# Performance work log

Measured on AMD Instinct MI355X. Metric: run time of the kernel, lower is better.

Reference implementation:

```python
import jax, jax.numpy as jnp
import numpy as np

B, N, D, HID, OUT = 4, 6144, 64, 512, 64
FINE_CONF = 0.25


def setup_inputs() -> dict:
    key = jax.random.key(0)
    ks = jax.random.split(key, 16)

    def unit(k, shape):
        v = jax.random.normal(k, shape, dtype=jnp.float32)
        return v / jnp.linalg.norm(v, axis=-1, keepdims=True)

    def lin(k, fan_in, shape):
        return jax.random.normal(k, shape, dtype=jnp.float32) * (1.0 / np.sqrt(fan_in))

    return {
        'feats1': unit(ks[0], (B, N, D)),
        'feats2': unit(ks[1], (B, N, D)),
        'kps1': jax.random.uniform(ks[2], (B, N, 2), dtype=jnp.float32) * 512.0,
        'kps2': jax.random.uniform(ks[3], (B, N, 2), dtype=jnp.float32) * 512.0,
        'scales1': jnp.ones((B, N), dtype=jnp.float32),
        'w1': lin(ks[4], 2 * D, (2 * D, HID)), 'b1': jnp.zeros((HID,), jnp.float32),
        'w2': lin(ks[5], HID, (HID, HID)),   'b2': jnp.zeros((HID,), jnp.float32),
        'w3': lin(ks[6], HID, (HID, HID)),   'b3': jnp.zeros((HID,), jnp.float32),
        'w4': lin(ks[7], HID, (HID, HID)),   'b4': jnp.zeros((HID,), jnp.float32),
        'w5': lin(ks[8], HID, (HID, OUT)),   'b5': jnp.zeros((OUT,), jnp.float32),
    }


def _fine_matcher(x, w1, b1, w2, b2, w3, b3, w4, b4, w5, b5):
    # eval-mode BN folded into the Linears -> plain MLP
    h = jax.nn.relu(x @ w1 + b1)
    h = jax.nn.relu(h @ w2 + b2)
    h = jax.nn.relu(h @ w3 + b3)
    h = jax.nn.relu(h @ w4 + b4)
    return h @ w5 + b5  # [B, N, 64]


def reference(feats1, feats2, kps1, kps2, scales1,
              w1, b1, w2, b2, w3, b3, w4, b4, w5, b5):
    # ---- batch_match: dense cosine sim + bidirectional argmax + mutual check ----
    cossim = jnp.einsum('bnd,bmd->bnm', feats1, feats2)       # [B, N, N]
    match12 = jnp.argmax(cossim, axis=-1)                      # [B, N]
    match21 = jnp.argmax(cossim, axis=1)                       # [B, N] (argmax over rows)
    idx0 = jnp.arange(match12.shape[1])
    back = jnp.take_along_axis(match21, match12, axis=1)       # match21[match12]
    mutual = back == idx0[None, :]                             # [B, N] bool

    # ---- refine_matches (masked instead of boolean compaction, jit-friendly) ----
    f2 = jnp.take_along_axis(feats2, match12[..., None], axis=1)   # [B, N, D]
    mkpts1 = jnp.take_along_axis(kps2, match12[..., None], axis=1) # [B, N, 2]
    offsets_raw = _fine_matcher(jnp.concatenate([feats1, f2], axis=-1),
                                w1, b1, w2, b2, w3, b3, w4, b4, w5, b5)  # [B, N, 64]

    # conf = softmax(3*offsets).max ; subpix uses softmax(3*offsets) too (temp=3)
    heat = jax.nn.softmax(3.0 * offsets_raw, axis=-1)          # [B, N, 64]
    conf = jnp.max(heat, axis=-1)                              # [B, N]

    hm = heat.reshape(heat.shape[0], heat.shape[1], 8, 8)      # [B, N, Hh, Wh]
    g = jnp.arange(8, dtype=heat.dtype) - 4.0                  # x - W//2 / y - H//2
    coords_x = jnp.sum(hm * g[None, None, None, :], axis=(-1, -2))
    coords_y = jnp.sum(hm * g[None, None, :, None], axis=(-1, -2))
    offsets = jnp.stack([coords_x, coords_y], axis=-1)         # [B, N, 2]

    mkpts0 = kps1 + offsets * scales1[..., None]
    matches = jnp.concatenate([mkpts0, mkpts1], axis=-1)       # [B, N, 4]
    mask_good = mutual & (conf > FINE_CONF)                    # valid-match mask
    return matches, mask_good
```

## Files before the change

kernel.cpp:

```cpp
#include <hip/hip_runtime.h>
#include <cstddef>
#include <cstdint>

#define BB 4
#define NN 6144
#define DD 64
#define HID 512
#define OUTD 64
#define CAP 512
#define RSPLIT 8

typedef unsigned long long ull;
typedef unsigned int u32;
typedef unsigned short u16;
typedef unsigned char u8;
typedef __attribute__((ext_vector_type(8))) short short8_t;
typedef __attribute__((ext_vector_type(4))) float floatx4;

#define OFF_ROWFIN 0
#define OFF_COLFIN 196608
#define OFF_WT     393216
#define OFF_F1T    2162688
#define OFF_F2T    5308416
#define OFF_RBM    8454144
#define OFF_CBM    10813440
#define OFF_CNTR   13172736
#define OFF_CNTC   13173504
#define OFF_LISTR  13174272
#define OFF_LISTC  13567488

#define WT1_OFF 0
#define WT2_OFF 65536
#define WT3_OFF 327680
#define WT4_OFF 589824
#define WT5_OFF 851968
#define WT_TOTAL 884736

__device__ __forceinline__ unsigned int fkey(float v) {
    unsigned int u = __float_as_uint(v);
    return (u & 0x80000000u) ? ~u : (u | 0x80000000u);
}

__device__ __forceinline__ float inv16(u32 k16) {
    u32 u = k16 << 16;
    return (u & 0x80000000u) ? __uint_as_float(u & 0x7fffffffu)
                             : __uint_as_float(~u);
}

__device__ __forceinline__ u16 f2bf(float f) {
    unsigned int u = __float_as_uint(f);
    u += 0x7FFFu + ((u >> 16) & 1u);
    return (u16)(u >> 16);
}

__device__ __forceinline__ u32 f2fp8x2(float a, float b) {
    return (u32)__builtin_amdgcn_cvt_pk_fp8_f32(a, b, 0, false) & 0xffffu;
}

__global__ __launch_bounds__(256) void prep_kernel(
    const float* __restrict__ w1, const float* __restrict__ w2,
    const float* __restrict__ w3, const float* __restrict__ w4,
    const float* __restrict__ w5,
    const float* __restrict__ f1, const float* __restrict__ f2,
    u8* __restrict__ wt8, u16* __restrict__ f1t, u16* __restrict__ f2t,
    ull* __restrict__ finals, int* __restrict__ cnts)
{
    int idx = blockIdx.x * 256 + threadIdx.x;

    if (idx < 2 * BB * NN) finals[idx] = 0ULL;
    if (idx < 384) cnts[idx] = 0;

    if (idx < WT_TOTAL) {
        const float* w; u8* o; int K, nsh, li;
        if (idx < 65536)        { w = w1; o = wt8 + WT1_OFF; K = 128; nsh = 9; li = idx; }
        else if (idx < 327680)  { w = w2; o = wt8 + WT2_OFF; K = 512; nsh = 9; li = idx - 65536; }
        else if (idx < 589824)  { w = w3; o = wt8 + WT3_OFF; K = 512; nsh = 9; li = idx - 327680; }
        else if (idx < 851968)  { w = w4; o = wt8 + WT4_OFF; K = 512; nsh = 9; li = idx - 589824; }
        else                    { w = w5; o = wt8 + WT5_OFF; K = 512; nsh = 6; li = idx - 851968; }
        int k = li >> nsh;
        int n = li & ((1 << nsh) - 1);
        u8 v = (u8)(f2fp8x2(w[li], 0.0f) & 0xff);
        int lane = (n & 15) | (((k >> 3) & 3) << 4);
        o[(((size_t)(n >> 4) * (K >> 5) + (k >> 5)) * 64 + lane) * 8 + (k & 7)] = v;
    }

    {
        const int TE = BB * NN * DD;
        const float* src; u16* dst; int e;
        if (idx < TE) { src = f1; dst = f1t; e = idx; }
        else          { src = f2; dst = f2t; e = idx - TE; }
        int k  = e & 63;
        int rn = e >> 6;
        int b  = rn / NN;
        int r  = rn - b * NN;
        int R  = r >> 7, rb = (r >> 4) & 7;
        int kb = k >> 5, lane = (r & 15) | (((k >> 3) & 3) << 4), j = k & 7;
        dst[(size_t)(b * 48 + R) * 8192 + ((rb * 2 + kb) * 64 + lane) * 8 + j] = f2bf(src[e]);
    }
}

__global__ __launch_bounds__(256, 4) void simb_kernel(
    const u16* __restrict__ f1t, const u16* __restrict__ f2t,
    u16* __restrict__ rbm, u16* __restrict__ cbm)
{
    __shared__ __align__(16) u16 sA[8192];
    __shared__ __align__(16) u16 sB[8192];
    __shared__ float cv[4][128];
    const int R = blockIdx.x, C = blockIdx.y, b = blockIdx.z;
    const int t = threadIdx.x, lane = t & 63, w = t >> 6;
    const int l15 = lane & 15, l4 = lane >> 4;

    const u16* Ag = f1t + (size_t)(b * 48 + R) * 8192;
    const u16* Bg = f2t + (size_t)(b * 48 + C) * 8192;

    #pragma unroll
    for (int rnd = 0; rnd < 4; ++rnd) {
        int c = rnd * 256 + t;
        *reinterpret_cast<uint4*>(&sA[c * 8]) = *reinterpret_cast<const uint4*>(Ag + c * 8);
        *reinterpret_cast<uint4*>(&sB[c * 8]) = *reinterpret_cast<const uint4*>(Bg + c * 8);
    }
    __syncthreads();

    floatx4 acc[2][8];
    #pragma unroll
    for (int i = 0; i < 2; ++i)
        #pragma unroll
        for (int j = 0; j < 8; ++j) acc[i][j] = (floatx4)(0.0f);

    #pragma unroll
    for (int kb = 0; kb < 2; ++kb) {
        short8_t afr[2];
        #pragma unroll
        for (int i = 0; i < 2; ++i)
            afr[i] = *reinterpret_cast<const short8_t*>(
                &sA[(((2 * w + i) * 2 + kb) * 64 + lane) * 8]);
        #pragma unroll
        for (int j = 0; j < 8; ++j) {
            short8_t bfr = *reinterpret_cast<const short8_t*>(
                &sB[((j * 2 + kb) * 64 + lane) * 8]);
            #pragma unroll
            for (int i = 0; i < 2; ++i)
                acc[i][j] = __builtin_amdgcn_mfma_f32_16x16x32_bf16(
                    afr[i], bfr, acc[i][j], 0, 0, 0);
        }
    }

    #pragma unroll
    for (int i = 0; i < 2; ++i) {
        #pragma unroll
        for (int reg = 0; reg < 4; ++reg) {
            float v = acc[i][0][reg];
            #pragma unroll
            for (int j = 1; j < 8; ++j) v = fmaxf(v, acc[i][j][reg]);
            v = fmaxf(v, __shfl_xor(v, 1));
            v = fmaxf(v, __shfl_xor(v, 2));
            v = fmaxf(v, __shfl_xor(v, 4));
            v = fmaxf(v, __shfl_xor(v, 8));
            if (l15 == 0) {
                int row = R * 128 + w * 32 + i * 16 + l4 * 4 + reg;
                rbm[((size_t)b * 48 + C) * NN + row] = (u16)(fkey(v) >> 16);
            }
        }
    }

    #pragma unroll
    for (int j = 0; j < 8; ++j) {
        float v = acc[0][j][0];
        #pragma unroll
        for (int i = 0; i < 2; ++i)
            #pragma unroll
            for (int reg = 0; reg < 4; ++reg) v = fmaxf(v, acc[i][j][reg]);
        v = fmaxf(v, __shfl_xor(v, 16));
        v = fmaxf(v, __shfl_xor(v, 32));
        if (l4 == 0) cv[w][j * 16 + l15] = v;
    }
    __syncthreads();
    if (t < 128) {
        float v = fmaxf(fmaxf(cv[0][t], cv[1][t]), fmaxf(cv[2][t], cv[3][t]));
        cbm[((size_t)b * 48 + R) * NN + C * 128 + t] = (u16)(fkey(v) >> 16);
    }
}

__global__ __launch_bounds__(256) void scan_kernel(
    const u16* __restrict__ rbm, const u16* __restrict__ cbm,
    int* __restrict__ cntR, int* __restrict__ cntC,
    int* __restrict__ listR, int* __restrict__ listC)
{
    const u16* bm = blockIdx.y ? cbm : rbm;
    int* cnt  = blockIdx.y ? cntC : cntR;
    int* list = blockIdx.y ? listC : listR;

    __shared__ int lcnt[48];
    __shared__ int lbase[48];
    const int t = threadIdx.x;
    if (t < 48) lcnt[t] = 0;
    const int idx = blockIdx.x * 256 + t;
    const int b = (blockIdx.x * 256) / NN;
    const int n = idx - b * NN;

    u16 ks[48];
    #pragma unroll
    for (int c = 0; c < 48; ++c)
        ks[c] = bm[((size_t)b * 48 + c) * NN + n];

    u16 mx = 0;
    #pragma unroll
    for (int c = 0; c < 48; ++c) mx = ks[c] > mx ? ks[c] : mx;
    float thr = inv16(mx) - 0.010f;
    u32 m0 = 0, m1 = 0;
    #pragma unroll
    for (int c = 0; c < 48; ++c) {
        if (inv16((u32)ks[c] + 1) >= thr) {
            if (c < 32) m0 |= 1u << c; else m1 |= 1u << (c - 32);
        }
    }
    __syncthreads();
    {
        u32 a = m0;
        while (a) { int c = __builtin_ctz(a); a &= a - 1; atomicAdd(&lcnt[c], 1); }
        a = m1;
        while (a) { int c = 32 + __builtin_ctz(a); a &= a - 1; atomicAdd(&lcnt[c], 1); }
    }
    __syncthreads();
    if (t < 48) { lbase[t] = atomicAdd(&cnt[b * 48 + t], lcnt[t]); lcnt[t] = 0; }
    __syncthreads();
    {
        u32 a = m0;
        while (a) {
            int c = __builtin_ctz(a); a &= a - 1;
            int pos = lbase[c] + atomicAdd(&lcnt[c], 1);
            if (pos < CAP) list[(b * 48 + c) * CAP + pos] = n;
        }
        a = m1;
        while (a) {
            int c = 32 + __builtin_ctz(a); a &= a - 1;
            int pos = lbase[c] + atomicAdd(&lcnt[c], 1);
            if (pos < CAP) list[(b * 48 + c) * CAP + pos] = n;
        }
    }
}

__global__ __launch_bounds__(256, 2) void refine_kernel(
    const float* __restrict__ f1, const float* __restrict__ f2,
    const int* __restrict__ cntR, const int* __restrict__ cntC,
    const int* __restrict__ listR, const int* __restrict__ listC,
    ull* __restrict__ rowfin, ull* __restrict__ colfin)
{
    const float* qfeat = blockIdx.z ? f2 : f1;
    const float* tfeat = blockIdx.z ? f1 : f2;
    const int* cnt  = blockIdx.z ? cntC : cntR;
    const int* list = blockIdx.z ? listC : listR;
    ull* fin = blockIdx.z ? colfin : rowfin;

    const int b = blockIdx.x / 48;
    const int C = blockIdx.x - b * 48;
    const int sub = blockIdx.y;
    int n_items = cnt[b * 48 + C];
    if (n_items > CAP) n_items = CAP;
    int chunk = (n_items + RSPLIT - 1) / RSPLIT;
    int lo = sub * chunk;
    int hi = lo + chunk; if (hi > n_items) hi = n_items;
    if (lo >= hi) return;

    __shared__ float s2f[128 * 68];
    __shared__ float sq[16 * 68];
    const int t = threadIdx.x;
    const float* tb = tfeat + ((size_t)b * NN + C * 128) * 64;
    #pragma unroll
    for (int p = 0; p < 8; ++p) {
        int idx = p * 256 + t;
        int row = idx >> 4, c4 = idx & 15;
        *reinterpret_cast<float4*>(&s2f[row * 68 + c4 * 4]) =
            *reinterpret_cast<const float4*>(tb + row * 64 + c4 * 4);
    }
    __syncthreads();
    const int rs = t >> 4, cg = t & 15;
    const int* mylist = list + (b * 48 + C) * CAP;
    for (int base = lo; base < hi; base += 16) {
        {
            int lq = base + rs;
            int nn = (lq < hi) ? mylist[lq] : mylist[lo];
            *reinterpret_cast<float4*>(&sq[rs * 68 + cg * 4]) =
                *reinterpret_cast<const float4*>(qfeat + ((size_t)b * NN + nn) * 64 + cg * 4);
        }
        __syncthreads();

        int li = base + rs;
        bool valid = li < hi;
        int n = valid ? mylist[li] : mylist[lo];
        float dot[8];
        #pragma unroll
        for (int c8 = 0; c8 < 8; ++c8) dot[c8] = 0.0f;
        #pragma unroll 4
        for (int kq = 0; kq < 16; ++kq) {
            float4 a4 = *reinterpret_cast<const float4*>(&sq[rs * 68 + kq * 4]);
            #pragma unroll
            for (int c8 = 0; c8 < 8; ++c8) {
                float4 s4 = *reinterpret_cast<const float4*>(&s2f[(cg + 16 * c8) * 68 + kq * 4]);
                dot[c8] = fmaf(a4.x, s4.x, dot[c8]);
                dot[c8] = fmaf(a4.y, s4.y, dot[c8]);
                dot[c8] = fmaf(a4.z, s4.z, dot[c8]);
                dot[c8] = fmaf(a4.w, s4.w, dot[c8]);
            }
        }
        float bv = dot[0]; int bc = cg;
        #pragma unroll
        for (int c8 = 1; c8 < 8; ++c8) {
            if (dot[c8] > bv) { bv = dot[c8]; bc = cg + 16 * c8; }
        }
        ull pk = ((ull)fkey(bv) << 32) | (u32)(~(u32)(C * 128 + bc));
        ull qq;
        qq = __shfl_xor(pk, 1); pk = pk > qq ? pk : qq;
        qq = __shfl_xor(pk, 2); pk = pk > qq ? pk : qq;
        qq = __shfl_xor(pk, 4); pk = pk > qq ? pk : qq;
        qq = __shfl_xor(pk, 8); pk = pk > qq ? pk : qq;
        if (cg == 0 && valid) atomicMax(&fin[(size_t)b * NN + n], pk);
        __syncthreads();
    }
}


#define MLP_STEP(BUF, KB)                                                        \
    {                                                                            \
        const int kb2 = ((KB) + woff) & (NKB - 1);                               \
        __builtin_amdgcn_s_setprio(1);                                           \
        _Pragma("unroll")                                                        \
        for (int jb = 0; jb < 6; ++jb) {                                         \
            const int pt = jb * 16 + l15;                                        \
            const int sp = (kb2 * 4 + l4) ^ (pt & 7);                            \
            long bfr = *reinterpret_cast<const long*>(act + pt * 512 + sp * 8);  \
            _Pragma("unroll")                                                    \
            for (int ia = 0; ia < 4; ++ia)                                       \
                acc[ia][jb] = __builtin_amdgcn_mfma_f32_16x16x32_fp8_fp8(        \
                    BUF[ia], bfr, acc[ia][jb], 0, 0, 0);                         \
        }                                                                        \
        __builtin_amdgcn_s_setprio(0);                                           \
        if ((KB) + 3 < NKB) {                                                    \
            const int kbp = ((KB) + 3 + woff) & (NKB - 1);                       \
            _Pragma("unroll")                                                    \
            for (int ia = 0; ia < 4; ++ia)                                       \
                BUF[ia] = *reinterpret_cast<const long*>(                        \
                    wt8 + (((size_t)(chBlk0 + ia) * NKB + kbp) * 64 + lane) * 8);\
        }                                                                        \
    }

template<int K>
__device__ __forceinline__ void mlp_layer8(
    u8* act, const u8* __restrict__ wt8,
    const float* __restrict__ bias, int lane, int wid)
{
    constexpr int NKB = K / 32;
    floatx4 acc[4][6];
    #pragma unroll
    for (int ia = 0; ia < 4; ++ia)
        #pragma unroll
        for (int jb = 0; jb < 6; ++jb)
            acc[ia][jb] = (floatx4)(0.0f);

    const int l15 = lane & 15, l4 = lane >> 4;
    const int chBlk0 = wid * 4;
    const int woff = (wid * 2) & (NKB - 1);

    long a0[4], a1[4], a2[4];
    #pragma unroll
    for (int ia = 0; ia < 4; ++ia)
        a0[ia] = *reinterpret_cast<const long*>(
            wt8 + (((size_t)(chBlk0 + ia) * NKB + ((0 + woff) & (NKB - 1))) * 64 + lane) * 8);
    #pragma unroll
    for (int ia = 0; ia < 4; ++ia)
        a1[ia] = *reinterpret_cast<const long*>(
            wt8 + (((size_t)(chBlk0 + ia) * NKB + ((1 + woff) & (NKB - 1))) * 64 + lane) * 8);
    #pragma unroll
    for (int ia = 0; ia < 4; ++ia)
        a2[ia] = *reinterpret_cast<const long*>(
            wt8 + (((size_t)(chBlk0 + ia) * NKB + ((2 + woff) & (NKB - 1))) * 64 + lane) * 8);

    #pragma unroll
    for (int kb = 0; kb < NKB; ++kb) {
        if ((kb % 3) == 0)      MLP_STEP(a0, kb)
        else if ((kb % 3) == 1) MLP_STEP(a1, kb)
        else                    MLP_STEP(a2, kb)
    }
    __syncthreads();

    const int ch0 = wid * 64;
    #pragma unroll
    for (int ia = 0; ia < 4; ++ia) {
        int cb = ia * 16 + l4 * 4;
        float4 bv = *reinterpret_cast<const float4*>(bias + ch0 + cb);
        #pragma unroll
        for (int jb = 0; jb < 6; ++jb) {
            int pt = jb * 16 + l15;
            u32 pk0 = f2fp8x2(fmaxf(acc[ia][jb][0] + bv.x, 0.0f),
                              fmaxf(acc[ia][jb][1] + bv.y, 0.0f));
            u32 pk1 = f2fp8x2(fmaxf(acc[ia][jb][2] + bv.z, 0.0f),
                              fmaxf(acc[ia][jb][3] + bv.w, 0.0f));
            u32 word = pk0 | (pk1 << 16);
            int s = (ch0 + cb) >> 3;
            int sp = s ^ (pt & 7);
            *reinterpret_cast<u32*>(act + pt * 512 + sp * 8 + (cb & 4)) = word;
        }
    }
    __syncthreads();
}

__global__ __launch_bounds__(512, 2) void mlp_mfma_kernel(
    const float* __restrict__ f1, const float* __restrict__ f2,
    const float* __restrict__ kps1, const float* __restrict__ kps2,
    const float* __restrict__ scales1,
    const float* __restrict__ b1, const float* __restrict__ b2,
    const float* __restrict__ b3, const float* __restrict__ b4,
    const float* __restrict__ b5,
    const u8* __restrict__ wt8,
    const ull* __restrict__ rowfin, const ull* __restrict__ colfin,
    float* __restrict__ out)
{
    __shared__ __align__(16) unsigned char lds_raw[49152];
    u8* act = lds_raw;
    float* logf = reinterpret_cast<float*>(lds_raw);

    const int t = threadIdx.x;
    const int lane = t & 63, wid = t >> 6;
    const int base = blockIdx.x * 96;
    const int b = base / NN;
    const int n0 = base % NN;

    if (t < 384) {
        const int pt = t >> 2, seg = t & 3;
        const int n = n0 + pt;
        ull rm = rowfin[(size_t)b * NN + n];
        const int m = (int)(~(u32)(rm & 0xffffffffULL));
        const float* src = (seg < 2)
            ? (f1 + ((size_t)b * NN + n) * DD + seg * 32)
            : (f2 + ((size_t)b * NN + m) * DD + (seg - 2) * 32);
        #pragma unroll
        for (int q8 = 0; q8 < 4; ++q8) {
            float4 v0 = *reinterpret_cast<const float4*>(src + q8 * 8);
            float4 v1 = *reinterpret_cast<const float4*>(src + q8 * 8 + 4);
            ull w64 = (ull)f2fp8x2(v0.x, v0.y)
                    | ((ull)f2fp8x2(v0.z, v0.w) << 16)
                    | ((ull)f2fp8x2(v1.x, v1.y) << 32)
                    | ((ull)f2fp8x2(v1.z, v1.w) << 48);
            int s = seg * 4 + q8;
            int sp = s ^ (pt & 7);
            *reinterpret_cast<ull*>(act + pt * 512 + sp * 8) = w64;
        }
    }
    __syncthreads();

    mlp_layer8<128>(act, wt8 + WT1_OFF, b1, lane, wid);
    mlp_layer8<512>(act, wt8 + WT2_OFF, b2, lane, wid);
    mlp_layer8<512>(act, wt8 + WT3_OFF, b3, lane, wid);
    mlp_layer8<512>(act, wt8 + WT4_OFF, b4, lane, wid);

    {
        const int l15 = lane & 15, l4 = lane >> 4;
        floatx4 acc5[6];
        #pragma unroll
        for (int jb = 0; jb < 6; ++jb) acc5[jb] = (floatx4)(0.0f);
        if (wid < 4) {
            const int woff5 = (wid * 4) & 15;
            long a_cur = *reinterpret_cast<const long*>(
                wt8 + WT5_OFF + (((size_t)wid * 16 + woff5) * 64 + lane) * 8);
            long a_nxt;
            #pragma unroll
            for (int kb = 0; kb < 16; ++kb) {
                const int kb2 = (kb + woff5) & 15;
                if (kb + 1 < 16) {
                    const int kbn = (kb + 1 + woff5) & 15;
                    a_nxt = *reinterpret_cast<const long*>(
                        wt8 + WT5_OFF + (((size_t)wid * 16 + kbn) * 64 + lane) * 8);
                }
                __builtin_amdgcn_s_setprio(1);
                #pragma unroll
                for (int jb = 0; jb < 6; ++jb) {
                    const int pt = jb * 16 + l15;
                    const int sp = (kb2 * 4 + l4) ^ (pt & 7);
                    long bfr = *reinterpret_cast<const long*>(act + pt * 512 + sp * 8);
                    acc5[jb] = __builtin_amdgcn_mfma_f32_16x16x32_fp8_fp8(
                        a_cur, bfr, acc5[jb], 0, 0, 0);
                }
                __builtin_amdgcn_s_setprio(0);
                if (kb + 1 < 16) a_cur = a_nxt;
            }
        }
        __syncthreads();
        if (wid < 4) {
            int cb = wid * 16 + l4 * 4;
            float4 bv = *reinterpret_cast<const float4*>(b5 + cb);
            #pragma unroll
            for (int jb = 0; jb < 6; ++jb) {
                int pt = jb * 16 + l15;
                float4 o;
                o.x = acc5[jb][0] + bv.x;
                o.y = acc5[jb][1] + bv.y;
                o.z = acc5[jb][2] + bv.z;
                o.w = acc5[jb][3] + bv.w;
                *reinterpret_cast<float4*>(&logf[pt * 68 + cb]) = o;
            }
        }
        __syncthreads();
    }

    if (t < 96) {
        const int pt = t;
        const int n = n0 + pt;
        const float* lrow = &logf[pt * 68];
        float mx = -1e30f;
        #pragma unroll 8
        for (int j = 0; j < OUTD; ++j) mx = fmaxf(mx, 3.0f * lrow[j]);
        float s = 0.0f, cx = 0.0f, cy = 0.0f;
        #pragma unroll 8
        for (int j = 0; j < OUTD; ++j) {
            float e = __expf(3.0f * lrow[j] - mx);
            s  += e;
            cx += e * (float)((j & 7) - 4);
            cy += e * (float)((j >> 3) - 4);
        }
        float conf = 1.0f / s;
        cx /= s; cy /= s;
        ull rm = rowfin[(size_t)b * NN + n];
        int m = (int)(~(u32)(rm & 0xffffffffULL));
        ull cm = colfin[(size_t)b * NN + m];
        int back = (int)(~(u32)(cm & 0xffffffffULL));
        bool mutual = (back == n);
        float sc = scales1[(size_t)b * NN + n];
        float x0 = kps1[((size_t)b * NN + n) * 2 + 0] + cx * sc;
        float y0 = kps1[((size_t)b * NN + n) * 2 + 1] + cy * sc;
        float x1 = kps2[((size_t)b * NN + m) * 2 + 0];
        float y1 = kps2[((size_t)b * NN + m) * 2 + 1];
        float* mt = out + ((size_t)b * NN + n) * 4;
        mt[0] = x0; mt[1] = y0; mt[2] = x1; mt[3] = y1;
        out[(size_t)BB * NN * 4 + (size_t)b * NN + n] =
            (mutual && conf > 0.25f) ? 1.0f : 0.0f;
    }
}

extern "C" void kernel_launch(void* const* d_in, const int* in_sizes, int n_in,
                              void* d_out, int out_size, void* d_ws, size_t ws_size,
                              hipStream_t stream)
{
    const float* f1  = (const float*)d_in[0];
    const float* f2  = (const float*)d_in[1];
    const float* kp1 = (const float*)d_in[2];
    const float* kp2 = (const float*)d_in[3];
    const float* sc1 = (const float*)d_in[4];
    const float* w1  = (const float*)d_in[5];
    const float* b1  = (const float*)d_in[6];
    const float* w2  = (const float*)d_in[7];
    const float* b2  = (const float*)d_in[8];
    const float* w3  = (const float*)d_in[9];
    const float* b3  = (const float*)d_in[10];
    const float* w4  = (const float*)d_in[11];
    const float* b4  = (const float*)d_in[12];
    const float* w5  = (const float*)d_in[13];
    const float* b5  = (const float*)d_in[14];

    char* ws = (char*)d_ws;
    ull* rowfin = (ull*)(ws + OFF_ROWFIN);
    ull* colfin = (ull*)(ws + OFF_COLFIN);
    u8*  wt8    = (u8*)(ws + OFF_WT);
    u16* f1t    = (u16*)(ws + OFF_F1T);
    u16* f2t    = (u16*)(ws + OFF_F2T);
    u16* rbm    = (u16*)(ws + OFF_RBM);
    u16* cbm    = (u16*)(ws + OFF_CBM);
    int* cntR   = (int*)(ws + OFF_CNTR);
    int* cntC   = (int*)(ws + OFF_CNTC);
    int* listR  = (int*)(ws + OFF_LISTR);
    int* listC  = (int*)(ws + OFF_LISTC);
    float* out  = (float*)d_out;

    prep_kernel<<<(2 * BB * NN * DD) / 256, 256, 0, stream>>>(
        w1, w2, w3, w4, w5, f1, f2, wt8, f1t, f2t, rowfin, cntR);

    dim3 gS(48, 48, BB);
    simb_kernel<<<gS, 256, 0, stream>>>(f1t, f2t, rbm, cbm);

    dim3 gScan((BB * NN) / 256, 2);
    scan_kernel<<<gScan, 256, 0, stream>>>(rbm, cbm, cntR, cntC, listR, listC);

    dim3 gR(BB * 48, RSPLIT, 2);
    refine_kernel<<<gR, 256, 0, stream>>>(f1, f2, cntR, cntC, listR, listC,
                                          rowfin, colfin);

    mlp_mfma_kernel<<<(BB * NN) / 96, 512, 0, stream>>>(
        f1, f2, kp1, kp2, sc1, b1, b2, b3, b4, b5, wt8, rowfin, colfin, out);
}
```

Measured before the change: 139.9 us.

## Register-tile candidate refinement kernel and reduce row split factor

The refinement kernel, which recomputes exact fp32 argmax over a 128-column chunk for listed candidate rows, no longer stages the 128 target rows in shared memory. Each thread now computes a 4x4 register tile (4 queries by 4 targets), reading target vectors directly from global/L2, over 32 queries per iteration. RSPLIT drops from 8 to 2, so fewer blocks each handle more items and the per-block target load is amortized differently. This trades shared-memory staging and LDS bandwidth for more global loads of the target tile and fewer launched blocks, which may reduce parallelism.

```diff
diff --git a/kernel.cpp b/kernel.cpp
--- a/kernel.cpp
+++ b/kernel.cpp
@@ -8,7 +8,7 @@
 #define HID 512
 #define OUTD 64
 #define CAP 512
-#define RSPLIT 8
+#define RSPLIT 2
 
 typedef unsigned long long ull;
 typedef unsigned int u32;
@@ -262,60 +262,76 @@
     int hi = lo + chunk; if (hi > n_items) hi = n_items;
     if (lo >= hi) return;
 
-    __shared__ float s2f[128 * 68];
-    __shared__ float sq[16 * 68];
+    __shared__ float sq[32 * 64];
     const int t = threadIdx.x;
+    const int tq = t & 31;
+    const int qg = t >> 5;
     const float* tb = tfeat + ((size_t)b * NN + C * 128) * 64;
-    #pragma unroll
-    for (int p = 0; p < 8; ++p) {
-        int idx = p * 256 + t;
-        int row = idx >> 4, c4 = idx & 15;
-        *reinterpret_cast<float4*>(&s2f[row * 68 + c4 * 4]) =
-            *reinterpret_cast<const float4*>(tb + row * 64 + c4 * 4);
-    }
-    __syncthreads();
-    const int rs = t >> 4, cg = t & 15;
     const int* mylist = list + (b * 48 + C) * CAP;
-    for (int base = lo; base < hi; base += 16) {
-        {
-            int lq = base + rs;
+
+    for (int base = lo; base < hi; base += 32) {
+        __syncthreads();
+        #pragma unroll
+        for (int s = 0; s < 2; ++s) {
+            int fi = s * 256 + t;
+            int q = fi >> 4, c4 = fi & 15;
+            int lq = base + q;
             int nn = (lq < hi) ? mylist[lq] : mylist[lo];
-            *reinterpret_cast<float4*>(&sq[rs * 68 + cg * 4]) =
-                *reinterpret_cast<const float4*>(qfeat + ((size_t)b * NN + nn) * 64 + cg * 4);
+            *reinterpret_cast<float4*>(&sq[q * 64 + c4 * 4]) =
+                *reinterpret_cast<const float4*>(
+                    qfeat + ((size_t)b * NN + nn) * 64 + c4 * 4);
         }
         __syncthreads();
 
-        int li = base + rs;
-        bool valid = li < hi;
-        int n = valid ? mylist[li] : mylist[lo];
-        float dot[8];
-        #pragma unroll
-        for (int c8 = 0; c8 < 8; ++c8) dot[c8] = 0.0f;
+        float acc[4][4];
+        #pragma unroll
+        for (int j = 0; j < 4; ++j)
+            #pragma unroll
+            for (int i = 0; i < 4; ++i) acc[j][i] = 0.0f;
+
         #pragma unroll 4
         for (int kq = 0; kq < 16; ++kq) {
-            float4 a4 = *reinterpret_cast<const float4*>(&sq[rs * 68 + kq * 4]);
-            #pragma unroll
-            for (int c8 = 0; c8 < 8; ++c8) {
-                float4 s4 = *reinterpret_cast<const float4*>(&s2f[(cg + 16 * c8) * 68 + kq * 4]);
-                dot[c8] = fmaf(a4.x, s4.x, dot[c8]);
-                dot[c8] = fmaf(a4.y, s4.y, dot[c8]);
-                dot[c8] = fmaf(a4.z, s4.z, dot[c8]);
-                dot[c8] = fmaf(a4.w, s4.w, dot[c8]);
+            float4 qv[4];
+            #pragma unroll
+            for (int j = 0; j < 4; ++j)
+                qv[j] = *reinterpret_cast<const float4*>(
+                    &sq[(qg * 4 + j) * 64 + kq * 4]);
+            float4 tv[4];
+            #pragma unroll
+            for (int i = 0; i < 4; ++i)
+                tv[i] = *reinterpret_cast<const float4*>(
+                    tb + (tq * 4 + i) * 64 + kq * 4);
+            #pragma unroll
+            for (int j = 0; j < 4; ++j)
+                #pragma unroll
+                for (int i = 0; i < 4; ++i) {
+                    acc[j][i] = fmaf(qv[j].x, tv[i].x, acc[j][i]);
+                    acc[j][i] = fmaf(qv[j].y, tv[i].y, acc[j][i]);
+                    acc[j][i] = fmaf(qv[j].z, tv[i].z, acc[j][i]);
+                    acc[j][i] = fmaf(qv[j].w, tv[i].w, acc[j][i]);
+                }
+        }
+
+        #pragma unroll
+        for (int j = 0; j < 4; ++j) {
+            int lq = base + qg * 4 + j;
+            bool valid = lq < hi;
+            float bv = acc[j][0]; int bt = tq * 4;
+            #pragma unroll
+            for (int i = 1; i < 4; ++i)
+                if (acc[j][i] > bv) { bv = acc[j][i]; bt = tq * 4 + i; }
+            ull pk = ((ull)fkey(bv) << 32) | (u32)(~(u32)(C * 128 + bt));
+            ull qq;
+            qq = __shfl_xor(pk, 1);  pk = pk > qq ? pk : qq;
+            qq = __shfl_xor(pk, 2);  pk = pk > qq ? pk : qq;
+            qq = __shfl_xor(pk, 4);  pk = pk > qq ? pk : qq;
+            qq = __shfl_xor(pk, 8);  pk = pk > qq ? pk : qq;
+            qq = __shfl_xor(pk, 16); pk = pk > qq ? pk : qq;
+            if (tq == 0 && valid) {
+                int n = mylist[lq];
+                atomicMax(&fin[(size_t)b * NN + n], pk);
             }
         }
-        float bv = dot[0]; int bc = cg;
-        #pragma unroll
-        for (int c8 = 1; c8 < 8; ++c8) {
-            if (dot[c8] > bv) { bv = dot[c8]; bc = cg + 16 * c8; }
-        }
-        ull pk = ((ull)fkey(bv) << 32) | (u32)(~(u32)(C * 128 + bc));
-        ull qq;
-        qq = __shfl_xor(pk, 1); pk = pk > qq ? pk : qq;
-        qq = __shfl_xor(pk, 2); pk = pk > qq ? pk : qq;
-        qq = __shfl_xor(pk, 4); pk = pk > qq ? pk : qq;
-        qq = __shfl_xor(pk, 8); pk = pk > qq ? pk : qq;
-        if (cg == 0 && valid) atomicMax(&fin[(size_t)b * NN + n], pk);
-        __syncthreads();
     }
 }
 
```

New measurement: 193.4 us. 1.38x slower.
